# Kernel optimization log

Hardware: AMD Instinct MI355X
Metric: run time of the kernel (lower is better)

The kernel has to match this reference:

```python
import jax, jax.numpy as jnp
import numpy as np

N_NODES = 100000
IN_C, HID_C, OUT_C = 128, 128, 64
N_EDGES, N_POS, N_NEG = 1600000, 200000, 200000
BN_EPS = 1e-5


def setup_inputs() -> dict:
    key = jax.random.key(0)
    ks = jax.random.split(key, 24)
    s = 0.05
    inp = {
        'x': jax.random.normal(ks[0], (N_NODES, IN_C), jnp.float32),
        'edge_index': jax.random.randint(ks[1], (2, N_EDGES), 0, N_NODES, jnp.int64 if jax.config.jax_enable_x64 else jnp.int32),
        'pos_edge_index': jax.random.randint(ks[2], (2, N_POS), 0, N_NODES, jnp.int32),
        'neg_edge_index': jax.random.randint(ks[3], (2, N_NEG), 0, N_NODES, jnp.int32),
        # SAGEConv layer 1 (in->hid): lin_l (bias) on aggregated neighbors, lin_r (no bias) on root
        'Wl1': jax.random.normal(ks[4], (IN_C, HID_C), jnp.float32) * s,
        'bl1': jnp.zeros((HID_C,), jnp.float32),
        'Wr1': jax.random.normal(ks[5], (IN_C, HID_C), jnp.float32) * s,
        'g1': jnp.ones((HID_C,), jnp.float32),
        'b1': jnp.zeros((HID_C,), jnp.float32),
        # SAGEConv layer 2 (hid->hid)
        'Wl2': jax.random.normal(ks[6], (HID_C, HID_C), jnp.float32) * s,
        'bl2': jnp.zeros((HID_C,), jnp.float32),
        'Wr2': jax.random.normal(ks[7], (HID_C, HID_C), jnp.float32) * s,
        'g2': jnp.ones((HID_C,), jnp.float32),
        'b2': jnp.zeros((HID_C,), jnp.float32),
        # SAGEConv layer 3 (hid->out)
        'Wl3': jax.random.normal(ks[8], (HID_C, OUT_C), jnp.float32) * s,
        'bl3': jnp.zeros((OUT_C,), jnp.float32),
        'Wr3': jax.random.normal(ks[9], (HID_C, OUT_C), jnp.float32) * s,
        # edge predictor: Linear(2*out, hid) -> ReLU -> Linear(hid, 1)
        'We1': jax.random.normal(ks[10], (2 * OUT_C, HID_C), jnp.float32) * s,
        'be1': jnp.zeros((HID_C,), jnp.float32),
        'We2': jax.random.normal(ks[11], (HID_C, 1), jnp.float32) * s,
        'be2': jnp.zeros((1,), jnp.float32),
    }
    return inp


def _sage_conv(x, src, dst, Wl, bl, Wr):
    # mean aggregation of source features at destination nodes (PyG SAGEConv default)
    msg = x[src]                                                   # [E, C] gather
    agg = jax.ops.segment_sum(msg, dst, num_segments=N_NODES)      # [N, C] scatter-add
    deg = jax.ops.segment_sum(jnp.ones((src.shape[0],), x.dtype), dst, num_segments=N_NODES)
    mean = agg / jnp.maximum(deg, 1.0)[:, None]
    return mean @ Wl + bl + x @ Wr


def _bn_eval(x, gamma, beta):
    # BatchNorm1d eval mode with init running stats (mean 0, var 1)
    return x * (gamma / jnp.sqrt(1.0 + BN_EPS)) + beta


def _encode(x, edge_index, Wl1, bl1, Wr1, g1, b1, Wl2, bl2, Wr2, g2, b2, Wl3, bl3, Wr3):
    src, dst = edge_index[0], edge_index[1]
    h = x
    # layer 1 (+ residual: in_channels == hidden_channels)
    h1 = jax.nn.relu(_bn_eval(_sage_conv(h, src, dst, Wl1, bl1, Wr1), g1, b1))
    h = h1 + h if h.shape[1] == h1.shape[1] else h1
    # layer 2 (+ residual)
    h2 = jax.nn.relu(_bn_eval(_sage_conv(h, src, dst, Wl2, bl2, Wr2), g2, b2))
    h = h2 + h
    # output layer (no norm/relu/residual)
    return _sage_conv(h, src, dst, Wl3, bl3, Wr3)


def _decode(z, edge_index, We1, be1, We2, be2):
    s, d = edge_index[0], edge_index[1]
    ef = jnp.concatenate([z[s], z[d]], axis=-1)           # [E, 2*OUT_C]
    hidden = jax.nn.relu(ef @ We1 + be1)
    return jax.nn.sigmoid((hidden @ We2 + be2)[:, 0])


def reference(x, edge_index, pos_edge_index, neg_edge_index,
              Wl1, bl1, Wr1, g1, b1, Wl2, bl2, Wr2, g2, b2, Wl3, bl3, Wr3,
              We1, be1, We2, be2):
    z = _encode(x, edge_index, Wl1, bl1, Wr1, g1, b1, Wl2, bl2, Wr2, g2, b2, Wl3, bl3, Wr3)
    pos = _decode(z, pos_edge_index, We1, be1, We2, be2)
    neg = _decode(z, neg_edge_index, We1, be1, We2, be2)
    return (z, pos, neg)
```

## Files before the change

kernel.cpp:

```cpp
#include <hip/hip_runtime.h>
#include <hip/hip_bf16.h>

typedef unsigned short u16;
typedef short short8 __attribute__((ext_vector_type(8)));
typedef float floatx4 __attribute__((ext_vector_type(4)));

__device__ __forceinline__ float b2f(u16 u) {
    unsigned v = ((unsigned)u) << 16;
    float f;
    __builtin_memcpy(&f, &v, 4);
    return f;
}
__device__ __forceinline__ float b2f_lo(unsigned w) { return b2f((u16)(w & 0xffffu)); }
__device__ __forceinline__ float b2f_hi(unsigned w) { return b2f((u16)(w >> 16)); }
__device__ __forceinline__ u16 f2b(float f) {
    unsigned u;
    __builtin_memcpy(&u, &f, 4);
    u = u + 0x7fffu + ((u >> 16) & 1u);
    return (u16)(u >> 16);
}
__device__ __forceinline__ unsigned pack2(float a, float b) {
    return (unsigned)f2b(a) | ((unsigned)f2b(b) << 16);
}
__device__ __forceinline__ float loadp(const void* p, int i, int f) {
    return f ? ((const float*)p)[i] : b2f(((const u16*)p)[i]);
}
__device__ __forceinline__ void acc8(float* a, uint4 p) {
    a[0] += b2f_lo(p.x); a[1] += b2f_hi(p.x);
    a[2] += b2f_lo(p.y); a[3] += b2f_hi(p.y);
    a[4] += b2f_lo(p.z); a[5] += b2f_hi(p.z);
    a[6] += b2f_lo(p.w); a[7] += b2f_hi(p.w);
}

__global__ void sniff_kernel(const unsigned* __restrict__ xw, const int* __restrict__ eiw,
                             int* __restrict__ flags) {
    __shared__ int s_fp32, s_i64;
    if (threadIdx.x == 0) { s_fp32 = 0; s_i64 = 1; }
    __syncthreads();
    int t = threadIdx.x;
    unsigned w = xw[t];
    float lo = b2f_lo(w);
    if (!(fabsf(lo) <= 64.0f)) atomicOr(&s_fp32, 1);
    if (eiw[2 * t + 1] != 0) atomicAnd(&s_i64, 0);
    __syncthreads();
    if (t == 0) { flags[0] = s_fp32; flags[1] = s_i64; }
}

__global__ void cvt_x_kernel(const void* __restrict__ x, u16* __restrict__ xb,
                             const int* __restrict__ flags, int nPairs) {
    int f = flags[0];
    int i = blockIdx.x * 256 + threadIdx.x;
    if (i >= nPairs) return;
    unsigned* out = (unsigned*)xb;
    if (f) {
        float2 v = ((const float2*)x)[i];
        out[i] = pack2(v.x, v.y);
    } else {
        out[i] = ((const unsigned*)x)[i];
    }
}

__global__ void prep_all_kernel(const void* Wl1, const void* Wr1, u16* __restrict__ Wcat1,
                                const void* Wl2, const void* Wr2, u16* __restrict__ Wcat2,
                                const void* Wl3, const void* Wr3, u16* __restrict__ Wcat3,
                                const void* We1, u16* __restrict__ Web,
                                const void* g1, const void* b1, const void* bl1,
                                float* __restrict__ al1, float* __restrict__ bt1,
                                const void* g2, const void* b2, const void* bl2,
                                float* __restrict__ al2, float* __restrict__ bt2,
                                const void* bl3,
                                float* __restrict__ al3, float* __restrict__ bt3,
                                const void* be1, const void* We2, const void* be2,
                                float* __restrict__ dparams,
                                const int* __restrict__ flags) {
    int f = flags[0];
    int idx = blockIdx.x * 256 + threadIdx.x;
    if (idx < 16384) {
        Wcat1[idx] = f ? f2b(((const float*)Wl1)[idx]) : ((const u16*)Wl1)[idx];
        Wcat1[16384 + idx] = f ? f2b(((const float*)Wr1)[idx]) : ((const u16*)Wr1)[idx];
    } else if (idx < 32768) {
        int i = idx - 16384;
        Wcat2[i] = f ? f2b(((const float*)Wl2)[i]) : ((const u16*)Wl2)[i];
        Wcat2[16384 + i] = f ? f2b(((const float*)Wr2)[i]) : ((const u16*)Wr2)[i];
    } else if (idx < 49152) {
        int i = idx - 32768;
        int k = i >> 7, n = i & 127;
        const void* src = (n < 64) ? Wl3 : Wr3;
        int j = k * 64 + (n & 63);
        Wcat3[i] = f ? f2b(((const float*)src)[j]) : ((const u16*)src)[j];
    } else if (idx < 65536) {
        int i = idx - 49152;
        Web[i] = f ? f2b(((const float*)We1)[i]) : ((const u16*)We1)[i];
    } else {
        int i = idx - 65536;
        if (i < 128) {
            float s = loadp(g1, i, f) * rsqrtf(1.0f + 1e-5f);
            al1[i] = s;
            bt1[i] = loadp(bl1, i, f) * s + loadp(b1, i, f);
        } else if (i < 256) {
            int j = i - 128;
            float s = loadp(g2, j, f) * rsqrtf(1.0f + 1e-5f);
            al2[j] = s;
            bt2[j] = loadp(bl2, j, f) * s + loadp(b2, j, f);
        } else if (i < 384) {
            int j = i - 256;
            al3[j] = 1.0f;
            bt3[j] = (j < 64) ? 0.0f : loadp(bl3, j - 64, f);
        } else if (i < 512) {
            int j = i - 384;
            dparams[j] = loadp(be1, j, f);
            dparams[128 + j] = loadp(We2, j, f);
            if (j == 0) dparams[256] = loadp(be2, 0, f);
        }
    }
}

__device__ __forceinline__ int edge_at(const int* ei, long long idx, int i64) {
    return i64 ? ei[2 * idx] : ei[idx];
}

__global__ __launch_bounds__(256) void bucket_count_kernel(const int* __restrict__ ei,
                                                           int* __restrict__ blockhist,
                                                           int E, int EPB, int B1, int nbuck,
                                                           const int* __restrict__ flags) {
    __shared__ int hist[1024];
    for (int i = threadIdx.x; i < nbuck; i += 256) hist[i] = 0;
    __syncthreads();
    int i64 = flags[1];
    int b = blockIdx.x;
    int lo = b * EPB, hi = min(lo + EPB, E);
    for (int e = lo + (int)threadIdx.x; e < hi; e += 256) {
        int d = edge_at(ei, (long long)E + e, i64);
        atomicAdd(&hist[d >> 7], 1);
    }
    __syncthreads();
    for (int k = threadIdx.x; k < nbuck; k += 256)
        blockhist[(size_t)k * B1 + b] = hist[k];
}

__global__ __launch_bounds__(64) void colscan_kernel(int* __restrict__ blockhist,
                                                     int* __restrict__ coltot, int B1) {
    int k = blockIdx.x, l = threadIdx.x;
    int* bh = blockhist + (size_t)k * B1;
    int x0 = (l < B1) ? bh[l] : 0;
    int x1 = (64 + l < B1) ? bh[64 + l] : 0;
    int s0 = x0;
    #pragma unroll
    for (int off = 1; off < 64; off <<= 1) {
        int u = __shfl_up(s0, off, 64);
        if (l >= off) s0 += u;
    }
    int tot0 = __shfl(s0, 63, 64);
    int s1 = x1;
    #pragma unroll
    for (int off = 1; off < 64; off <<= 1) {
        int u = __shfl_up(s1, off, 64);
        if (l >= off) s1 += u;
    }
    int tot1 = __shfl(s1, 63, 64);
    s1 += tot0;
    if (l < B1) bh[l] = s0 - x0;
    if (64 + l < B1) bh[64 + l] = s1 - x1;
    if (l == 0) coltot[k] = tot0 + tot1;
}

__global__ __launch_bounds__(1024) void base_scan_kernel(const int* __restrict__ coltot,
                                                         int* __restrict__ bucketbase,
                                                         int* __restrict__ rowptrN,
                                                         int nbuck, int E) {
    __shared__ int wsum[16];
    int t = threadIdx.x, lane = t & 63, w = t >> 6;
    int v = (t < nbuck) ? coltot[t] : 0;
    int inc = v;
    #pragma unroll
    for (int off = 1; off < 64; off <<= 1) {
        int u = __shfl_up(inc, off, 64);
        if (lane >= off) inc += u;
    }
    if (lane == 63) wsum[w] = inc;
    __syncthreads();
    int add = 0;
    for (int i = 0; i < w; ++i) add += wsum[i];
    if (t < nbuck) bucketbase[t] = add + inc - v;
    if (t == 0) rowptrN[0] = E;
}

__global__ __launch_bounds__(256) void bucket_scatter_kernel(const int* __restrict__ ei,
                                                             const int* __restrict__ bucketbase,
                                                             const int* __restrict__ blockhist,
                                                             int2* __restrict__ pairs,
                                                             int E, int EPB, int B1, int nbuck,
                                                             const int* __restrict__ flags) {
    __shared__ int off[1024];
    int b = blockIdx.x;
    for (int k = threadIdx.x; k < nbuck; k += 256)
        off[k] = bucketbase[k] + blockhist[(size_t)k * B1 + b];
    __syncthreads();
    int i64 = flags[1];
    int lo = b * EPB, hi = min(lo + EPB, E);
    for (int e = lo + (int)threadIdx.x; e < hi; e += 256) {
        int s = edge_at(ei, e, i64);
        int d = edge_at(ei, (long long)E + e, i64);
        int slot = atomicAdd(&off[d >> 7], 1);
        pairs[slot] = make_int2(s, d);
    }
}

__global__ __launch_bounds__(256) void bucket_csr_kernel(const int2* __restrict__ pairs,
                                                         const int* __restrict__ bucketbase,
                                                         const int* __restrict__ coltot,
                                                         int* __restrict__ rowptr,
                                                         int* __restrict__ col, int N) {
    __shared__ int srcs[4096];
    __shared__ unsigned char dl[4096];
    __shared__ int hist[128], cur[128];
    int k = blockIdx.x, tid = threadIdx.x;
    if (tid < 128) hist[tid] = 0;
    __syncthreads();
    int base = bucketbase[k], cnt = coltot[k];
    int staged = min(cnt, 4096);
    for (int i = tid; i < cnt; i += 256) {
        int2 pr = pairs[base + i];
        int j = pr.y & 127;
        atomicAdd(&hist[j], 1);
        if (i < 4096) { srcs[i] = pr.x; dl[i] = (unsigned char)j; }
    }
    __syncthreads();
    if (tid < 64) {
        int x0 = hist[tid], x1 = hist[64 + tid];
        int s0 = x0;
        #pragma unroll
        for (int off = 1; off < 64; off <<= 1) {
            int u = __shfl_up(s0, off, 64);
            if (tid >= off) s0 += u;
        }
        int tot0 = __shfl(s0, 63, 64);
        int s1 = x1;
        #pragma unroll
        for (int off = 1; off < 64; off <<= 1) {
            int u = __shfl_up(s1, off, 64);
            if (tid >= off) s1 += u;
        }
        s1 += tot0;
        cur[tid] = s0 - x0;
        cur[64 + tid] = s1 - x1;
    }
    __syncthreads();
    int node0 = k << 7;
    if (tid < 128 && node0 + tid < N) rowptr[node0 + tid] = base + cur[tid];
    __syncthreads();
    for (int i = tid; i < staged; i += 256) {
        int slot = base + atomicAdd(&cur[dl[i]], 1);
        col[slot] = srcs[i];
    }
    for (int i = 4096 + tid; i < cnt; i += 256) {
        int2 pr = pairs[base + i];
        int slot = base + atomicAdd(&cur[pr.y & 127], 1);
        col[slot] = pr.x;
    }
}

template <int CD>
__global__ __launch_bounds__(256) void aggregate_kernel(const u16* __restrict__ X,
                                                        const int* __restrict__ rowptr,
                                                        const int* __restrict__ col,
                                                        u16* __restrict__ meanout, int N) {
    constexpr int LPR = CD / 4;
    constexpr int GPB = 256 / LPR;
    int t = threadIdx.x;
    int g = t / LPR;
    int o = t % LPR;
    int u = blockIdx.x * GPB + g;
    if (u >= N) return;
    const uint4* Xv = (const uint4*)X;
    int beg = rowptr[u], end = rowptr[u + 1];
    float a[8] = {0.f, 0.f, 0.f, 0.f, 0.f, 0.f, 0.f, 0.f};
    int e = beg;
    for (; e + 4 <= end; e += 4) {
        int c0 = col[e], c1 = col[e + 1], c2 = col[e + 2], c3 = col[e + 3];
        uint4 p0 = Xv[(size_t)c0 * LPR + o];
        uint4 p1 = Xv[(size_t)c1 * LPR + o];
        uint4 p2 = Xv[(size_t)c2 * LPR + o];
        uint4 p3 = Xv[(size_t)c3 * LPR + o];
        acc8(a, p0); acc8(a, p1); acc8(a, p2); acc8(a, p3);
    }
    for (; e < end; ++e) {
        uint4 p = Xv[(size_t)col[e] * LPR + o];
        acc8(a, p);
    }
    int deg = end - beg;
    float inv = (deg > 0) ? 1.0f / (float)deg : 0.0f;
    uint4 ov;
    ov.x = pack2(a[0] * inv, a[1] * inv);
    ov.y = pack2(a[2] * inv, a[3] * inv);
    ov.z = pack2(a[4] * inv, a[5] * inv);
    ov.w = pack2(a[6] * inv, a[7] * inv);
    ((uint4*)meanout)[(size_t)u * LPR + o] = ov;
}

#define LDSA 40
__global__ __launch_bounds__(256) void gemm_sage_kernel(
    const u16* __restrict__ A1, const u16* __restrict__ A2,
    const u16* __restrict__ W, int N,
    const float* __restrict__ alpha, const float* __restrict__ beta,
    int addRes, u16* __restrict__ out, int ldo, u16* __restrict__ outB,
    int M, int K, int relu) {
    __shared__ u16 As[64 * LDSA];
    __shared__ u16 Wt[64 * LDSA];
    int tid = threadIdx.x;
    int mBase = blockIdx.x * 64, nBase = blockIdx.y * 64;
    int lane = tid & 63, w = tid >> 6;
    int wm = w >> 1, wn = w & 1;
    int q = lane >> 4, r = lane & 15;

    floatx4 acc[2][2];
    #pragma unroll
    for (int mi = 0; mi < 2; ++mi)
        #pragma unroll
        for (int ni = 0; ni < 2; ++ni)
            acc[mi][ni] = (floatx4){0.f, 0.f, 0.f, 0.f};

    for (int k0 = 0; k0 < K; k0 += 32) {
        const u16* Abase = (k0 < 128) ? (A1 + k0) : (A2 + (k0 - 128));
        {
            int row = tid >> 2, kc = (tid & 3) * 8;
            int gr = mBase + row;
            short8 v = (short8){0, 0, 0, 0, 0, 0, 0, 0};
            if (gr < M) v = *(const short8*)(Abase + (size_t)gr * 128 + kc);
            *(short8*)(&As[row * LDSA + kc]) = v;
        }
        {
            int kk = tid >> 3, nc = (tid & 7) * 8;
            short8 v = *(const short8*)(W + (size_t)(k0 + kk) * N + nBase + nc);
            #pragma unroll
            for (int j = 0; j < 8; ++j) Wt[(nc + j) * LDSA + kk] = ((u16*)&v)[j];
        }
        __syncthreads();
        short8 af[2], bfv[2];
        #pragma unroll
        for (int mi = 0; mi < 2; ++mi)
            af[mi] = *(const short8*)(&As[(wm * 32 + mi * 16 + r) * LDSA + q * 8]);
        #pragma unroll
        for (int ni = 0; ni < 2; ++ni)
            bfv[ni] = *(const short8*)(&Wt[(wn * 32 + ni * 16 + r) * LDSA + q * 8]);
        #pragma unroll
        for (int mi = 0; mi < 2; ++mi)
            #pragma unroll
            for (int ni = 0; ni < 2; ++ni)
                acc[mi][ni] = __builtin_amdgcn_mfma_f32_16x16x32_bf16(af[mi], bfv[ni], acc[mi][ni], 0, 0, 0);
        __syncthreads();
    }

    #pragma unroll
    for (int mi = 0; mi < 2; ++mi)
        #pragma unroll
        for (int ni = 0; ni < 2; ++ni) {
            int colv = nBase + wn * 32 + ni * 16 + r;
            float al = alpha[colv], be = beta[colv];
            #pragma unroll
            for (int r4 = 0; r4 < 4; ++r4) {
                int row = mBase + wm * 32 + mi * 16 + q * 4 + r4;
                if (row < M) {
                    float v = acc[mi][ni][r4] * al + be;
                    if (relu) v = fmaxf(v, 0.0f);
                    if (addRes) v += b2f(A2[(size_t)row * 128 + colv]);
                    if (outB) {
                        if (colv < 64) out[(size_t)row * ldo + colv] = f2b(v);
                        else outB[(size_t)row * 64 + (colv - 64)] = f2b(v);
                    } else {
                        out[(size_t)row * ldo + colv] = f2b(v);
                    }
                }
            }
        }
}

__global__ void combine_z_kernel(const u16* __restrict__ m, const u16* __restrict__ uu,
                                 u16* __restrict__ zbuf, void* __restrict__ dout,
                                 int nPairs, const int* __restrict__ flags) {
    int f = flags[0];
    int i = blockIdx.x * 256 + threadIdx.x;
    if (i >= nPairs) return;
    unsigned a = ((const unsigned*)m)[i];
    unsigned b = ((const unsigned*)uu)[i];
    float lo = b2f_lo(a) + b2f_lo(b);
    float hi = b2f_hi(a) + b2f_hi(b);
    unsigned zp = pack2(lo, hi);
    ((unsigned*)zbuf)[i] = zp;
    if (f) {
        float2 v; v.x = lo; v.y = hi;
        ((float2*)dout)[i] = v;
    } else {
        ((unsigned*)dout)[i] = zp;
    }
}

__global__ __launch_bounds__(256) void decode_kernel(
    const u16* __restrict__ z,
    const int* __restrict__ sidx, const int* __restrict__ didx,
    const u16* __restrict__ Web,
    const float* __restrict__ dparams,
    void* __restrict__ dout, long long outBase, int nE,
    const int* __restrict__ flags) {
    __shared__ u16 Wt[128 * 136];
    __shared__ u16 As[64 * 136];
    __shared__ float red[4][32];
    __shared__ float be1f[128], We2f[128];
    int tid = threadIdx.x;
    int f = flags[0];

    {
        int k = tid >> 1, nc0 = (tid & 1) * 64;
        #pragma unroll
        for (int c = 0; c < 8; ++c) {
            short8 v = *(const short8*)(Web + k * 128 + nc0 + c * 8);
            #pragma unroll
            for (int j = 0; j < 8; ++j) Wt[(nc0 + c * 8 + j) * 136 + k] = ((u16*)&v)[j];
        }
    }
    if (tid < 128) { be1f[tid] = dparams[tid]; We2f[tid] = dparams[128 + tid]; }

    int eBase = blockIdx.x * 64;
    {
        int row = tid >> 2, ch = tid & 3;
        int e = eBase + row;
        if (e >= nE) e = nE - 1;
        int node = (ch < 2) ? sidx[e] : didx[e];
        int off = (ch & 1) * 32;
        const short8* src = (const short8*)(z + (size_t)node * 64 + off);
        #pragma unroll
        for (int j = 0; j < 4; ++j)
            *(short8*)(&As[row * 136 + ch * 32 + j * 8]) = src[j];
    }
    __syncthreads();

    int lane = tid & 63, w = tid >> 6;
    int wm = w >> 1, wn = w & 1;
    int q = lane >> 4, r = lane & 15;
    floatx4 acc[2][4];
    #pragma unroll
    for (int mi = 0; mi < 2; ++mi)
        #pragma unroll
        for (int ni = 0; ni < 4; ++ni)
            acc[mi][ni] = (floatx4){0.f, 0.f, 0.f, 0.f};

    #pragma unroll
    for (int k0 = 0; k0 < 128; k0 += 32) {
        short8 af[2], bfv[4];
        #pragma unroll
        for (int mi = 0; mi < 2; ++mi)
            af[mi] = *(const short8*)(&As[(wm * 32 + mi * 16 + r) * 136 + k0 + q * 8]);
        #pragma unroll
        for (int ni = 0; ni < 4; ++ni)
            bfv[ni] = *(const short8*)(&Wt[(wn * 64 + ni * 16 + r) * 136 + k0 + q * 8]);
        #pragma unroll
        for (int mi = 0; mi < 2; ++mi)
            #pragma unroll
            for (int ni = 0; ni < 4; ++ni)
                acc[mi][ni] = __builtin_amdgcn_mfma_f32_16x16x32_bf16(af[mi], bfv[ni], acc[mi][ni], 0, 0, 0);
    }

    float part[2][4] = {{0.f, 0.f, 0.f, 0.f}, {0.f, 0.f, 0.f, 0.f}};
    #pragma unroll
    for (int mi = 0; mi < 2; ++mi)
        #pragma unroll
        for (int ni = 0; ni < 4; ++ni) {
            int colv = wn * 64 + ni * 16 + r;
            float bb = be1f[colv], mm = We2f[colv];
            #pragma unroll
            for (int r4 = 0; r4 < 4; ++r4) {
                float v = acc[mi][ni][r4] + bb;
                part[mi][r4] += fmaxf(v, 0.0f) * mm;
            }
        }
    #pragma unroll
    for (int mi = 0; mi < 2; ++mi)
        #pragma unroll
        for (int r4 = 0; r4 < 4; ++r4) {
            float v = part[mi][r4];
            v += __shfl_xor(v, 1, 64);
            v += __shfl_xor(v, 2, 64);
            v += __shfl_xor(v, 4, 64);
            v += __shfl_xor(v, 8, 64);
            part[mi][r4] = v;
        }
    if (r == 0) {
        #pragma unroll
        for (int mi = 0; mi < 2; ++mi)
            #pragma unroll
            for (int r4 = 0; r4 < 4; ++r4)
                red[w][mi * 16 + q * 4 + r4] = part[mi][r4];
    }
    __syncthreads();
    if (tid < 64) {
        int e = eBase + tid;
        if (e < nE) {
            int half = tid >> 5, loc = tid & 31;
            float s = red[half * 2 + 0][loc] + red[half * 2 + 1][loc] + dparams[256];
            float sg = 1.0f / (1.0f + expf(-s));
            if (f) ((float*)dout)[outBase + e] = sg;
            else   ((u16*)dout)[outBase + e] = f2b(sg);
        }
    }
}


extern "C" void kernel_launch(void* const* d_in, const int* in_sizes, int n_in,
                              void* d_out, int out_size, void* d_ws, size_t ws_size,
                              hipStream_t stream) {
    const void* x   = d_in[0];
    const int* ei   = (const int*)d_in[1];
    const int* pos  = (const int*)d_in[2];
    const int* neg  = (const int*)d_in[3];
    const void* Wl1 = d_in[4];
    const void* bl1 = d_in[5];
    const void* Wr1 = d_in[6];
    const void* g1  = d_in[7];
    const void* b1  = d_in[8];
    const void* Wl2 = d_in[9];
    const void* bl2 = d_in[10];
    const void* Wr2 = d_in[11];
    const void* g2  = d_in[12];
    const void* b2  = d_in[13];
    const void* Wl3 = d_in[14];
    const void* bl3 = d_in[15];
    const void* Wr3 = d_in[16];
    const void* We1 = d_in[17];
    const void* be1 = d_in[18];
    const void* We2 = d_in[19];
    const void* be2 = d_in[20];

    const int N = in_sizes[0] / 128;
    const int E = in_sizes[1] / 2;
    const int nPos = in_sizes[2] / 2;
    const int nNeg = in_sizes[3] / 2;
    const int nbuck = (N + 127) >> 7;
    const int EPB = (((E + 95) / 96) + 3) & ~3;
    const int B1 = (E + EPB - 1) / EPB;

    char* p = (char*)d_ws;
    auto alloc = [&](size_t bytes) -> void* {
        void* r = (void*)p;
        p += (bytes + 255) & ~(size_t)255;
        return r;
    };
    int*   flags     = (int*)alloc(64);
    int*   blockhist = (int*)alloc((size_t)nbuck * B1 * 4);
    int*   coltot    = (int*)alloc((size_t)nbuck * 4);
    int*   bucketbase= (int*)alloc((size_t)nbuck * 4);
    int*   rowptr    = (int*)alloc((size_t)(N + 1) * 4);
    int2*  pairs     = (int2*)alloc((size_t)E * 8);
    int*   colbuf    = (int*)alloc((size_t)E * 4);
    u16*   xb      = (u16*)alloc((size_t)N * 128 * 2);
    u16*   hbufA   = (u16*)alloc((size_t)N * 128 * 2);
    u16*   meanbuf = (u16*)alloc((size_t)N * 128 * 2);
    u16*   Wcat1   = (u16*)alloc((size_t)256 * 128 * 2);
    u16*   Wcat2   = (u16*)alloc((size_t)256 * 128 * 2);
    u16*   Wcat3   = (u16*)alloc((size_t)128 * 128 * 2);
    u16*   Web     = (u16*)alloc((size_t)128 * 128 * 2);
    float* al1 = (float*)alloc(128 * 4);
    float* bt1 = (float*)alloc(128 * 4);
    float* al2 = (float*)alloc(128 * 4);
    float* bt2 = (float*)alloc(128 * 4);
    float* al3 = (float*)alloc(128 * 4);
    float* bt3 = (float*)alloc(128 * 4);
    float* dparams = (float*)alloc(260 * 4);
    u16* hbufB = xb;
    u16* tbuf  = meanbuf;
    u16* ubuf  = meanbuf + (size_t)N * 64;
    u16* mbuf  = hbufA;
    u16* zbuf  = hbufA + (size_t)N * 64;

    sniff_kernel<<<1, 256, 0, stream>>>((const unsigned*)x, ei, flags);
    bucket_count_kernel<<<B1, 256, 0, stream>>>(ei, blockhist, E, EPB, B1, nbuck, flags);
    colscan_kernel<<<nbuck, 64, 0, stream>>>(blockhist, coltot, B1);
    base_scan_kernel<<<1, 1024, 0, stream>>>(coltot, bucketbase, rowptr + N, nbuck, E);
    bucket_scatter_kernel<<<B1, 256, 0, stream>>>(ei, bucketbase, blockhist, pairs, E, EPB, B1, nbuck, flags);
    bucket_csr_kernel<<<nbuck, 256, 0, stream>>>(pairs, bucketbase, coltot, rowptr, colbuf, N);

    cvt_x_kernel<<<(N * 64 + 255) / 256, 256, 0, stream>>>(x, xb, flags, N * 64);
    prep_all_kernel<<<(66048 + 255) / 256, 256, 0, stream>>>(
        Wl1, Wr1, Wcat1, Wl2, Wr2, Wcat2, Wl3, Wr3, Wcat3, We1, Web,
        g1, b1, bl1, al1, bt1, g2, b2, bl2, al2, bt2, bl3, al3, bt3,
        be1, We2, be2, dparams, flags);

    dim3 gemmGrid2((N + 63) / 64, 2);
    int aggGrid64 = (N + 15) / 16;
    int aggGrid32 = (N + 31) / 32;

    aggregate_kernel<64><<<aggGrid64, 256, 0, stream>>>(xb, rowptr, colbuf, meanbuf, N);
    gemm_sage_kernel<<<gemmGrid2, 256, 0, stream>>>(meanbuf, xb, Wcat1, 128, al1, bt1,
                                                    1, hbufA, 128, nullptr, N, 256, 1);
    aggregate_kernel<64><<<aggGrid64, 256, 0, stream>>>(hbufA, rowptr, colbuf, meanbuf, N);
    gemm_sage_kernel<<<gemmGrid2, 256, 0, stream>>>(meanbuf, hbufA, Wcat2, 128, al2, bt2,
                                                    1, hbufB, 128, nullptr, N, 256, 1);
    gemm_sage_kernel<<<gemmGrid2, 256, 0, stream>>>(hbufB, hbufB, Wcat3, 128, al3, bt3,
                                                    0, tbuf, 64, ubuf, N, 128, 0);
    aggregate_kernel<32><<<aggGrid32, 256, 0, stream>>>(tbuf, rowptr, colbuf, mbuf, N);
    combine_z_kernel<<<(N * 32 + 255) / 256, 256, 0, stream>>>(mbuf, ubuf, zbuf, d_out, N * 32, flags);

    long long posBase = (long long)N * 64;
    long long negBase = posBase + nPos;
    decode_kernel<<<(nPos + 63) / 64, 256, 0, stream>>>(zbuf, pos, pos + nPos, Web, dparams,
                                                        d_out, posBase, nPos, flags);
    decode_kernel<<<(nNeg + 63) / 64, 256, 0, stream>>>(zbuf, neg, neg + nNeg, Web, dparams,
                                                        d_out, negBase, nNeg, flags);
}
```

Baseline: 540.1 us.

## Gather neighbor features in FP8 and fuse final aggregation with z combine

Node features used in the three neighbor-mean aggregations are now stored as FP8 e4m3 copies, written by the conversion kernel and by the GEMM epilogues, which halves the bytes gathered per edge. The aggregation kernels decode FP8 to float and write bf16 means. The last aggregation is merged with the z combine step, so the separate combine kernel and its intermediate buffer disappear. This adds extra FP8 writes and reduces the precision of the aggregated inputs, which may push the output past the accuracy tolerance.

Measured after the change: 494.0 us. 1.09x faster.

```diff
diff --git a/kernel.cpp b/kernel.cpp
--- a/kernel.cpp
+++ b/kernel.cpp
@@ -2,8 +2,10 @@
 #include <hip/hip_bf16.h>
 
 typedef unsigned short u16;
+typedef unsigned char u8;
 typedef short short8 __attribute__((ext_vector_type(8)));
 typedef float floatx4 __attribute__((ext_vector_type(4)));
+typedef float floatx2 __attribute__((ext_vector_type(2)));
 
 __device__ __forceinline__ float b2f(u16 u) {
     unsigned v = ((unsigned)u) << 16;
@@ -25,11 +27,20 @@
 __device__ __forceinline__ float loadp(const void* p, int i, int f) {
     return f ? ((const float*)p)[i] : b2f(((const u16*)p)[i]);
 }
-__device__ __forceinline__ void acc8(float* a, uint4 p) {
-    a[0] += b2f_lo(p.x); a[1] += b2f_hi(p.x);
-    a[2] += b2f_lo(p.y); a[3] += b2f_hi(p.y);
-    a[4] += b2f_lo(p.z); a[5] += b2f_hi(p.z);
-    a[6] += b2f_lo(p.w); a[7] += b2f_hi(p.w);
+__device__ __forceinline__ u8 f2e4m3(float v) {
+    int r = __builtin_amdgcn_cvt_pk_fp8_f32(v, v, 0, false);
+    return (u8)(r & 0xff);
+}
+__device__ __forceinline__ void acc16_fp8(float* a, uint4 p) {
+    floatx2 f;
+    f = __builtin_amdgcn_cvt_pk_f32_fp8((int)p.x, false); a[0] += f[0];  a[1] += f[1];
+    f = __builtin_amdgcn_cvt_pk_f32_fp8((int)p.x, true);  a[2] += f[0];  a[3] += f[1];
+    f = __builtin_amdgcn_cvt_pk_f32_fp8((int)p.y, false); a[4] += f[0];  a[5] += f[1];
+    f = __builtin_amdgcn_cvt_pk_f32_fp8((int)p.y, true);  a[6] += f[0];  a[7] += f[1];
+    f = __builtin_amdgcn_cvt_pk_f32_fp8((int)p.z, false); a[8] += f[0];  a[9] += f[1];
+    f = __builtin_amdgcn_cvt_pk_f32_fp8((int)p.z, true);  a[10] += f[0]; a[11] += f[1];
+    f = __builtin_amdgcn_cvt_pk_f32_fp8((int)p.w, false); a[12] += f[0]; a[13] += f[1];
+    f = __builtin_amdgcn_cvt_pk_f32_fp8((int)p.w, true);  a[14] += f[0]; a[15] += f[1];
 }
 
 __global__ void sniff_kernel(const unsigned* __restrict__ xw, const int* __restrict__ eiw,
@@ -47,17 +58,23 @@
 }
 
 __global__ void cvt_x_kernel(const void* __restrict__ x, u16* __restrict__ xb,
+                             u16* __restrict__ x8,
                              const int* __restrict__ flags, int nPairs) {
     int f = flags[0];
     int i = blockIdx.x * 256 + threadIdx.x;
     if (i >= nPairs) return;
-    unsigned* out = (unsigned*)xb;
+    float lo, hi;
     if (f) {
         float2 v = ((const float2*)x)[i];
-        out[i] = pack2(v.x, v.y);
+        lo = v.x; hi = v.y;
+        ((unsigned*)xb)[i] = pack2(lo, hi);
     } else {
-        out[i] = ((const unsigned*)x)[i];
-    }
+        unsigned w = ((const unsigned*)x)[i];
+        lo = b2f_lo(w); hi = b2f_hi(w);
+        ((unsigned*)xb)[i] = w;
+    }
+    int r = __builtin_amdgcn_cvt_pk_fp8_f32(lo, hi, 0, false);
+    x8[i] = (u16)(r & 0xffff);
 }
 
 __global__ void prep_all_kernel(const void* Wl1, const void* Wr1, u16* __restrict__ Wcat1,
@@ -260,21 +277,23 @@
     }
 }
 
-template <int CD>
-__global__ __launch_bounds__(256) void aggregate_kernel(const u16* __restrict__ X,
-                                                        const int* __restrict__ rowptr,
-                                                        const int* __restrict__ col,
-                                                        u16* __restrict__ meanout, int N) {
-    constexpr int LPR = CD / 4;
+template <int CH>
+__global__ __launch_bounds__(256) void aggregate_fp8_kernel(const u8* __restrict__ X8,
+                                                            const int* __restrict__ rowptr,
+                                                            const int* __restrict__ col,
+                                                            u16* __restrict__ meanout, int N) {
+    constexpr int LPR = CH / 16;
     constexpr int GPB = 256 / LPR;
     int t = threadIdx.x;
     int g = t / LPR;
     int o = t % LPR;
     int u = blockIdx.x * GPB + g;
     if (u >= N) return;
-    const uint4* Xv = (const uint4*)X;
+    const uint4* Xv = (const uint4*)X8;
     int beg = rowptr[u], end = rowptr[u + 1];
-    float a[8] = {0.f, 0.f, 0.f, 0.f, 0.f, 0.f, 0.f, 0.f};
+    float a[16];
+    #pragma unroll
+    for (int i = 0; i < 16; ++i) a[i] = 0.f;
     int e = beg;
     for (; e + 4 <= end; e += 4) {
         int c0 = col[e], c1 = col[e + 1], c2 = col[e + 2], c3 = col[e + 3];
@@ -282,20 +301,85 @@
         uint4 p1 = Xv[(size_t)c1 * LPR + o];
         uint4 p2 = Xv[(size_t)c2 * LPR + o];
         uint4 p3 = Xv[(size_t)c3 * LPR + o];
-        acc8(a, p0); acc8(a, p1); acc8(a, p2); acc8(a, p3);
+        acc16_fp8(a, p0); acc16_fp8(a, p1); acc16_fp8(a, p2); acc16_fp8(a, p3);
     }
     for (; e < end; ++e) {
         uint4 p = Xv[(size_t)col[e] * LPR + o];
-        acc8(a, p);
+        acc16_fp8(a, p);
     }
     int deg = end - beg;
     float inv = (deg > 0) ? 1.0f / (float)deg : 0.0f;
-    uint4 ov;
-    ov.x = pack2(a[0] * inv, a[1] * inv);
-    ov.y = pack2(a[2] * inv, a[3] * inv);
-    ov.z = pack2(a[4] * inv, a[5] * inv);
-    ov.w = pack2(a[6] * inv, a[7] * inv);
-    ((uint4*)meanout)[(size_t)u * LPR + o] = ov;
+    uint4 ov0, ov1;
+    ov0.x = pack2(a[0] * inv, a[1] * inv);   ov0.y = pack2(a[2] * inv, a[3] * inv);
+    ov0.z = pack2(a[4] * inv, a[5] * inv);   ov0.w = pack2(a[6] * inv, a[7] * inv);
+    ov1.x = pack2(a[8] * inv, a[9] * inv);   ov1.y = pack2(a[10] * inv, a[11] * inv);
+    ov1.z = pack2(a[12] * inv, a[13] * inv); ov1.w = pack2(a[14] * inv, a[15] * inv);
+    uint4* mo = (uint4*)meanout;
+    mo[(size_t)u * (CH / 8) + o * 2 + 0] = ov0;
+    mo[(size_t)u * (CH / 8) + o * 2 + 1] = ov1;
+}
+
+__global__ __launch_bounds__(256) void agg_combine_kernel(const u8* __restrict__ T8,
+                                                          const int* __restrict__ rowptr,
+                                                          const int* __restrict__ col,
+                                                          const u16* __restrict__ ubuf,
+                                                          u16* __restrict__ zbuf,
+                                                          void* __restrict__ dout,
+                                                          int N, const int* __restrict__ flags) {
+    constexpr int LPR = 4;
+    constexpr int GPB = 64;
+    int f = flags[0];
+    int t = threadIdx.x;
+    int g = t / LPR;
+    int o = t % LPR;
+    int u = blockIdx.x * GPB + g;
+    if (u >= N) return;
+    const uint4* Xv = (const uint4*)T8;
+    int beg = rowptr[u], end = rowptr[u + 1];
+    float a[16];
+    #pragma unroll
+    for (int i = 0; i < 16; ++i) a[i] = 0.f;
+    int e = beg;
+    for (; e + 4 <= end; e += 4) {
+        int c0 = col[e], c1 = col[e + 1], c2 = col[e + 2], c3 = col[e + 3];
+        uint4 p0 = Xv[(size_t)c0 * LPR + o];
+        uint4 p1 = Xv[(size_t)c1 * LPR + o];
+        uint4 p2 = Xv[(size_t)c2 * LPR + o];
+        uint4 p3 = Xv[(size_t)c3 * LPR + o];
+        acc16_fp8(a, p0); acc16_fp8(a, p1); acc16_fp8(a, p2); acc16_fp8(a, p3);
+    }
+    for (; e < end; ++e) {
+        uint4 p = Xv[(size_t)col[e] * LPR + o];
+        acc16_fp8(a, p);
+    }
+    int deg = end - beg;
+    float inv = (deg > 0) ? 1.0f / (float)deg : 0.0f;
+    const uint4* uv = (const uint4*)(ubuf + (size_t)u * 64 + o * 16);
+    uint4 u0 = uv[0], u1 = uv[1];
+    float z[16];
+    z[0] = a[0] * inv + b2f_lo(u0.x);  z[1] = a[1] * inv + b2f_hi(u0.x);
+    z[2] = a[2] * inv + b2f_lo(u0.y);  z[3] = a[3] * inv + b2f_hi(u0.y);
+    z[4] = a[4] * inv + b2f_lo(u0.z);  z[5] = a[5] * inv + b2f_hi(u0.z);
+    z[6] = a[6] * inv + b2f_lo(u0.w);  z[7] = a[7] * inv + b2f_hi(u0.w);
+    z[8] = a[8] * inv + b2f_lo(u1.x);  z[9] = a[9] * inv + b2f_hi(u1.x);
+    z[10] = a[10] * inv + b2f_lo(u1.y); z[11] = a[11] * inv + b2f_hi(u1.y);
+    z[12] = a[12] * inv + b2f_lo(u1.z); z[13] = a[13] * inv + b2f_hi(u1.z);
+    z[14] = a[14] * inv + b2f_lo(u1.w); z[15] = a[15] * inv + b2f_hi(u1.w);
+    uint4 zv0, zv1;
+    zv0.x = pack2(z[0], z[1]);   zv0.y = pack2(z[2], z[3]);
+    zv0.z = pack2(z[4], z[5]);   zv0.w = pack2(z[6], z[7]);
+    zv1.x = pack2(z[8], z[9]);   zv1.y = pack2(z[10], z[11]);
+    zv1.z = pack2(z[12], z[13]); zv1.w = pack2(z[14], z[15]);
+    uint4* zo = (uint4*)(zbuf + (size_t)u * 64 + o * 16);
+    zo[0] = zv0; zo[1] = zv1;
+    if (f) {
+        float* fo = (float*)dout + (size_t)u * 64 + o * 16;
+        #pragma unroll
+        for (int i = 0; i < 16; ++i) fo[i] = z[i];
+    } else {
+        uint4* bo = (uint4*)((u16*)dout + (size_t)u * 64 + o * 16);
+        bo[0] = zv0; bo[1] = zv1;
+    }
 }
 
 #define LDSA 40
@@ -304,6 +388,7 @@
     const u16* __restrict__ W, int N,
     const float* __restrict__ alpha, const float* __restrict__ beta,
     int addRes, u16* __restrict__ out, int ldo, u16* __restrict__ outB,
+    u8* __restrict__ out8, int ld8,
     int M, int K, int relu) {
     __shared__ u16 As[64 * LDSA];
     __shared__ u16 Wt[64 * LDSA];
@@ -365,34 +450,15 @@
                     if (relu) v = fmaxf(v, 0.0f);
                     if (addRes) v += b2f(A2[(size_t)row * 128 + colv]);
                     if (outB) {
-                        if (colv < 64) out[(size_t)row * ldo + colv] = f2b(v);
+                        if (colv < 64) out8[(size_t)row * 64 + colv] = f2e4m3(v);
                         else outB[(size_t)row * 64 + (colv - 64)] = f2b(v);
                     } else {
                         out[(size_t)row * ldo + colv] = f2b(v);
+                        if (out8) out8[(size_t)row * ld8 + colv] = f2e4m3(v);
                     }
                 }
             }
         }
-}
-
-__global__ void combine_z_kernel(const u16* __restrict__ m, const u16* __restrict__ uu,
-                                 u16* __restrict__ zbuf, void* __restrict__ dout,
-                                 int nPairs, const int* __restrict__ flags) {
-    int f = flags[0];
-    int i = blockIdx.x * 256 + threadIdx.x;
-    if (i >= nPairs) return;
-    unsigned a = ((const unsigned*)m)[i];
-    unsigned b = ((const unsigned*)uu)[i];
-    float lo = b2f_lo(a) + b2f_lo(b);
-    float hi = b2f_hi(a) + b2f_hi(b);
-    unsigned zp = pack2(lo, hi);
-    ((unsigned*)zbuf)[i] = zp;
-    if (f) {
-        float2 v; v.x = lo; v.y = hi;
-        ((float2*)dout)[i] = v;
-    } else {
-        ((unsigned*)dout)[i] = zp;
-    }
 }
 
 __global__ __launch_bounds__(256) void decode_kernel(
@@ -554,6 +620,9 @@
     u16*   xb      = (u16*)alloc((size_t)N * 128 * 2);
     u16*   hbufA   = (u16*)alloc((size_t)N * 128 * 2);
     u16*   meanbuf = (u16*)alloc((size_t)N * 128 * 2);
+    u8*    x8      = (u8*)alloc((size_t)N * 128);
+    u8*    h8      = (u8*)alloc((size_t)N * 128);
+    u8*    t8      = (u8*)alloc((size_t)N * 64);
     u16*   Wcat1   = (u16*)alloc((size_t)256 * 128 * 2);
     u16*   Wcat2   = (u16*)alloc((size_t)256 * 128 * 2);
     u16*   Wcat3   = (u16*)alloc((size_t)128 * 128 * 2);
@@ -566,9 +635,7 @@
     float* bt3 = (float*)alloc(128 * 4);
     float* dparams = (float*)alloc(260 * 4);
     u16* hbufB = xb;
-    u16* tbuf  = meanbuf;
     u16* ubuf  = meanbuf + (size_t)N * 64;
-    u16* mbuf  = hbufA;
     u16* zbuf  = hbufA + (size_t)N * 64;
 
     sniff_kernel<<<1, 256, 0, stream>>>((const unsigned*)x, ei, flags);
@@ -578,26 +645,24 @@
     bucket_scatter_kernel<<<B1, 256, 0, stream>>>(ei, bucketbase, blockhist, pairs, E, EPB, B1, nbuck, flags);
     bucket_csr_kernel<<<nbuck, 256, 0, stream>>>(pairs, bucketbase, coltot, rowptr, colbuf, N);
 
-    cvt_x_kernel<<<(N * 64 + 255) / 256, 256, 0, stream>>>(x, xb, flags, N * 64);
+    cvt_x_kernel<<<(N * 64 + 255) / 256, 256, 0, stream>>>(x, xb, (u16*)x8, flags, N * 64);
     prep_all_kernel<<<(66048 + 255) / 256, 256, 0, stream>>>(
         Wl1, Wr1, Wcat1, Wl2, Wr2, Wcat2, Wl3, Wr3, Wcat3, We1, Web,
         g1, b1, bl1, al1, bt1, g2, b2, bl2, al2, bt2, bl3, al3, bt3,
         be1, We2, be2, dparams, flags);
 
     dim3 gemmGrid2((N + 63) / 64, 2);
-    int aggGrid64 = (N + 15) / 16;
-    int aggGrid32 = (N + 31) / 32;
-
-    aggregate_kernel<64><<<aggGrid64, 256, 0, stream>>>(xb, rowptr, colbuf, meanbuf, N);
+
+    aggregate_fp8_kernel<128><<<(N + 31) / 32, 256, 0, stream>>>(x8, rowptr, colbuf, meanbuf, N);
     gemm_sage_kernel<<<gemmGrid2, 256, 0, stream>>>(meanbuf, xb, Wcat1, 128, al1, bt1,
-                                                    1, hbufA, 128, nullptr, N, 256, 1);
-    aggregate_kernel<64><<<aggGrid64, 256, 0, stream>>>(hbufA, rowptr, colbuf, meanbuf, N);
+                                                    1, hbufA, 128, nullptr, h8, 128, N, 256, 1);
+    aggregate_fp8_kernel<128><<<(N + 31) / 32, 256, 0, stream>>>(h8, rowptr, colbuf, meanbuf, N);
     gemm_sage_kernel<<<gemmGrid2, 256, 0, stream>>>(meanbuf, hbufA, Wcat2, 128, al2, bt2,
-                                                    1, hbufB, 128, nullptr, N, 256, 1);
+                                                    1, hbufB, 128, nullptr, nullptr, 0, N, 256, 1);
     gemm_sage_kernel<<<gemmGrid2, 256, 0, stream>>>(hbufB, hbufB, Wcat3, 128, al3, bt3,
-                                                    0, tbuf, 64, ubuf, N, 128, 0);
-    aggregate_kernel<32><<<aggGrid32, 256, 0, stream>>>(tbuf, rowptr, colbuf, mbuf, N);
-    combine_z_kernel<<<(N * 32 + 255) / 256, 256, 0, stream>>>(mbuf, ubuf, zbuf, d_out, N * 32, flags);
+                                                    0, nullptr, 0, ubuf, t8, 64, N, 128, 0);
+    agg_combine_kernel<<<(N + 63) / 64, 256, 0, stream>>>(t8, rowptr, colbuf, ubuf, zbuf,
+                                                          d_out, N, flags);
 
     long long posBase = (long long)N * 64;
     long long negBase = posBase + nPos;
```
